# Optimization experiments

Measured on AMD Instinct MI355X. Metric: run time of the kernel, lower is better.

Reference implementation:

```python
import jax, jax.numpy as jnp
import numpy as np

B, T, C, H = 2, 2048, 1024, 16
HS = C // H  # 64
EPS = 1e-5


def layernorm(x, g, b):
    mu = jnp.mean(x, axis=-1, keepdims=True)
    var = jnp.var(x, axis=-1, keepdims=True)
    return (x - mu) * jax.lax.rsqrt(var + EPS) * g + b


def setup_inputs() -> dict:
    key = jax.random.key(0)
    ks = jax.random.split(key, 12)
    s = lambda fan_in: 1.0 / np.sqrt(fan_in)
    inp = {
        'x':  jax.random.normal(ks[0], (B, T, C), dtype=jnp.float32),
        'Wq': jax.random.uniform(ks[1], (H, C, HS), jnp.float32, -s(C), s(C)),
        'Wk': jax.random.uniform(ks[2], (H, C, HS), jnp.float32, -s(C), s(C)),
        'Wv': jax.random.uniform(ks[3], (H, C, HS), jnp.float32, -s(C), s(C)),
        'Wp': jax.random.uniform(ks[4], (C, C), jnp.float32, -s(C), s(C)),
        'bp': jax.random.uniform(ks[5], (C,), jnp.float32, -s(C), s(C)),
        'W1': jax.random.uniform(ks[6], (C, 4 * C), jnp.float32, -s(C), s(C)),
        'b1': jax.random.uniform(ks[7], (4 * C,), jnp.float32, -s(C), s(C)),
        'W2': jax.random.uniform(ks[8], (4 * C, C), jnp.float32, -s(4 * C), s(4 * C)),
        'b2': jax.random.uniform(ks[9], (C,), jnp.float32, -s(4 * C), s(4 * C)),
        'g1': jnp.ones((C,), jnp.float32),
        'be1': jnp.zeros((C,), jnp.float32),
        'g2': jnp.ones((C,), jnp.float32),
        'be2': jnp.zeros((C,), jnp.float32),
    }
    return inp


def block(x, Wq, Wk, Wv, Wp, bp, W1, b1, W2, b2, g1, be1, g2, be2):
    # quirky residual structure: residual is taken from the post-LN tensor
    x = layernorm(x, g1, be1)
    # batched multi-head attention (all heads at once): [B,H,T,HS]
    q = jnp.einsum('btc,hcd->bhtd', x, Wq)
    k = jnp.einsum('btc,hcd->bhtd', x, Wk)
    v = jnp.einsum('btc,hcd->bhtd', x, Wv)
    # NOTE: original scales by full embedding dim C ** -0.5, not head_size
    scores = jnp.einsum('bhtd,bhsd->bhts', q, k) * (C ** -0.5)
    causal = jnp.tril(jnp.ones((T, T), dtype=bool))
    scores = jnp.where(causal, scores, -jnp.inf)
    wei = jax.nn.softmax(scores, axis=-1)  # dropout p=0 in eval
    out = jnp.einsum('bhts,bhsd->bhtd', wei, v)
    out = out.transpose(0, 2, 1, 3).reshape(B, T, C)  # concat heads
    out = out @ Wp + bp
    x = x + out
    x = layernorm(x, g2, be2)
    ff = jax.nn.relu(x @ W1 + b1) @ W2 + b2
    return x + ff


def reference(x, Wq, Wk, Wv, Wp, bp, W1, b1, W2, b2, g1, be1, g2, be2):
    return block(x, Wq, Wk, Wv, Wp, bp, W1, b1, W2, b2, g1, be1, g2, be2)
```

## Files before the change

kernel.cpp:

```cpp
#include <hip/hip_runtime.h>
#include <hip/hip_bf16.h>
#include <cstdint>
#include <cstddef>

typedef __attribute__((ext_vector_type(8))) short short8;
typedef __attribute__((ext_vector_type(4))) float f32x4;
typedef __attribute__((ext_vector_type(16))) float f32x16;
typedef unsigned int u32;
typedef unsigned short u16;

__device__ inline u16 f2b(float x) {
    union { float f; u32 u; } v; v.f = x;
    u32 u = v.u;
    u32 r = (u + 0x7fff + ((u >> 16) & 1)) >> 16;
    return (u16)r;
}
__device__ inline float b2f(u16 h) {
    union { u32 u; float f; } v; v.u = ((u32)h) << 16;
    return v.f;
}
__device__ inline u32 cvtpk(float lo, float hi) {
    u32 r; asm("v_cvt_pk_bf16_f32 %0, %1, %2" : "=v"(r) : "v"(lo), "v"(hi)); return r;
}
__device__ inline float ex2(float x) {
    float r; asm("v_exp_f32 %0, %1" : "=v"(r) : "v"(x)); return r;
}
__device__ inline void gll16(const void* g, void* l) {
    __builtin_amdgcn_global_load_lds(
        (const __attribute__((address_space(1))) void*)g,
        (__attribute__((address_space(3))) void*)l, 16, 0, 0);
}

__global__ __launch_bounds__(256) void repack_qkv_tiled(
    const float* __restrict__ Wq, const float* __restrict__ Wk, const float* __restrict__ Wv,
    u16* __restrict__ out)
{
    __shared__ u16 lds[64 * 72];
    const int tid = threadIdx.x;
    const int c0 = blockIdx.x * 64;
    const int sh = blockIdx.y;
    const int sel = sh >> 4, h = sh & 15;
    const float* W = (sel == 0) ? Wq : (sel == 1) ? Wk : Wv;
    #pragma unroll
    for (int it = 0; it < 4; ++it) {
        int idx = tid + it * 256;
        int c = idx >> 4, d4 = idx & 15;
        float4 v = *reinterpret_cast<const float4*>(&W[((size_t)(h * 1024 + c0 + c)) * 64 + d4 * 4]);
        lds[(d4 * 4 + 0) * 72 + c] = f2b(v.x);
        lds[(d4 * 4 + 1) * 72 + c] = f2b(v.y);
        lds[(d4 * 4 + 2) * 72 + c] = f2b(v.z);
        lds[(d4 * 4 + 3) * 72 + c] = f2b(v.w);
    }
    __syncthreads();
    #pragma unroll
    for (int it = 0; it < 2; ++it) {
        int idx = tid + it * 256;
        int d = idx >> 3, c8 = idx & 7;
        short8 s = *reinterpret_cast<const short8*>(&lds[d * 72 + c8 * 8]);
        *reinterpret_cast<short8*>(&out[((size_t)(sel * 1024 + h * 64 + d)) * 1024 + c0 + c8 * 8]) = s;
    }
}

__global__ __launch_bounds__(256) void trans_tiled(
    const float* __restrict__ in, u16* __restrict__ out, int P, int Q)
{
    __shared__ u16 lds[64 * 72];
    const int tid = threadIdx.x;
    const int p0 = blockIdx.x * 64, q0 = blockIdx.y * 64;
    #pragma unroll
    for (int it = 0; it < 4; ++it) {
        int idx = tid + it * 256;
        int p = idx >> 4, q4 = idx & 15;
        float4 v = *reinterpret_cast<const float4*>(&in[(size_t)(p0 + p) * Q + q0 + q4 * 4]);
        lds[(q4 * 4 + 0) * 72 + p] = f2b(v.x);
        lds[(q4 * 4 + 1) * 72 + p] = f2b(v.y);
        lds[(q4 * 4 + 2) * 72 + p] = f2b(v.z);
        lds[(q4 * 4 + 3) * 72 + p] = f2b(v.w);
    }
    __syncthreads();
    #pragma unroll
    for (int it = 0; it < 2; ++it) {
        int idx = tid + it * 256;
        int q = idx >> 3, p8 = idx & 7;
        short8 s = *reinterpret_cast<const short8*>(&lds[q * 72 + p8 * 8]);
        *reinterpret_cast<short8*>(&out[(size_t)(q0 + q) * P + p0 + p8 * 8]) = s;
    }
}

__global__ __launch_bounds__(256) void vt_kernel(
    const u16* __restrict__ qkv, u16* __restrict__ vt)
{
    __shared__ u16 lds[64 * 72];
    const int tid = threadIdx.x;
    const int s0 = blockIdx.x * 64, h = blockIdx.y, b = blockIdx.z;
    #pragma unroll
    for (int it = 0; it < 2; ++it) {
        int idx = tid + it * 256;
        int s = idx >> 3, d8 = idx & 7;
        short8 kv = *reinterpret_cast<const short8*>(
            &qkv[((size_t)(b * 2048 + s0 + s)) * 3072 + 2048 + h * 64 + d8 * 8]);
        #pragma unroll
        for (int j = 0; j < 8; ++j) lds[(d8 * 8 + j) * 72 + s] = (u16)kv[j];
    }
    __syncthreads();
    #pragma unroll
    for (int it = 0; it < 2; ++it) {
        int idx = tid + it * 256;
        int d = idx >> 3, s8 = idx & 7;
        short8 s = *reinterpret_cast<const short8*>(&lds[d * 72 + s8 * 8]);
        *reinterpret_cast<short8*>(&vt[((size_t)(b * 16 + h) * 64 + d) * 2048 + s0 + s8 * 8]) = s;
    }
}

__global__ __launch_bounds__(256) void ln_kernel(
    const float* __restrict__ x, const float* __restrict__ g, const float* __restrict__ be,
    float* __restrict__ yf, u16* __restrict__ yb)
{
    int row = blockIdx.x;
    const float4 v = reinterpret_cast<const float4*>(x + (size_t)row * 1024)[threadIdx.x];
    float s  = v.x + v.y + v.z + v.w;
    float s2 = v.x * v.x + v.y * v.y + v.z * v.z + v.w * v.w;
    #pragma unroll
    for (int o = 32; o >= 1; o >>= 1) { s += __shfl_xor(s, o); s2 += __shfl_xor(s2, o); }
    __shared__ float red[8];
    int w = threadIdx.x >> 6;
    if ((threadIdx.x & 63) == 0) { red[w] = s; red[4 + w] = s2; }
    __syncthreads();
    s  = red[0] + red[1] + red[2] + red[3];
    s2 = red[4] + red[5] + red[6] + red[7];
    float mu = s * (1.0f / 1024.0f);
    float var = s2 * (1.0f / 1024.0f) - mu * mu;
    float rs = rsqrtf(var + 1e-5f);
    const float4 gg = reinterpret_cast<const float4*>(g)[threadIdx.x];
    const float4 bb = reinterpret_cast<const float4*>(be)[threadIdx.x];
    float4 o;
    o.x = (v.x - mu) * rs * gg.x + bb.x;
    o.y = (v.y - mu) * rs * gg.y + bb.y;
    o.z = (v.z - mu) * rs * gg.z + bb.z;
    o.w = (v.w - mu) * rs * gg.w + bb.w;
    reinterpret_cast<float4*>(yf + (size_t)row * 1024)[threadIdx.x] = o;
    uint2 pk;
    pk.x = (u32)f2b(o.x) | ((u32)f2b(o.y) << 16);
    pk.y = (u32)f2b(o.z) | ((u32)f2b(o.w) << 16);
    reinterpret_cast<uint2*>(yb + (size_t)row * 1024)[threadIdx.x] = pk;
}

template<bool BIAS, bool RELU, bool RESID, bool OUTB>
__global__ __launch_bounds__(256) void gemm_bt(
    const u16* __restrict__ A, int lda,
    const u16* __restrict__ BT, int ldb,
    void* __restrict__ out, int ldo,
    const float* __restrict__ bias,
    const float* __restrict__ resid,
    int K)
{
    __shared__ __align__(16) char smem[64 * 1024];
    const int tid = threadIdx.x;
    const int lane = tid & 63, w = tid >> 6;
    const int wr = w >> 1, wc = w & 1;
    const int l15 = lane & 15, lq = lane >> 4;

    const int nx = gridDim.x;
    const int nwg = nx * gridDim.y;
    int orig = blockIdx.y * nx + blockIdx.x;
    int wgid = orig;
    if ((nwg & 7) == 0) wgid = (orig & 7) * (nwg >> 3) + (orig >> 3);
    const int m0 = (wgid / nx) * 128, n0 = (wgid % nx) * 128;

    auto stage = [&](int kt, int buf) {
        char* As = smem + buf * 32768;
        char* Bs = smem + buf * 32768 + 16384;
        #pragma unroll
        for (int it = 0; it < 4; ++it) {
            int slot = it * 256 + tid;
            int row = slot >> 3, c8 = (slot & 7) ^ (row & 7);
            gll16(A + (size_t)(m0 + row) * lda + kt + c8 * 8, As + (it * 256 + w * 64) * 16);
        }
        #pragma unroll
        for (int it = 0; it < 4; ++it) {
            int slot = it * 256 + tid;
            int row = slot >> 3, c8 = (slot & 7) ^ (row & 7);
            gll16(BT + (size_t)(n0 + row) * ldb + kt + c8 * 8, Bs + (it * 256 + w * 64) * 16);
        }
    };

    f32x4 acc[4][4] = {};
    const int nk = K >> 6;

    stage(0, 0);
    __syncthreads();

    for (int t = 0; t < nk; ++t) {
        const char* As = smem + (t & 1) * 32768;
        const char* Bs = smem + (t & 1) * 32768 + 16384;
        if (t + 1 < nk) stage((t + 1) << 6, (t + 1) & 1);
        #pragma unroll
        for (int kk = 0; kk < 2; ++kk) {
            const int sc = kk * 4 + lq;
            short8 a[4], b[4];
            #pragma unroll
            for (int mi = 0; mi < 4; ++mi) {
                int row = wr * 64 + mi * 16 + l15;
                a[mi] = *reinterpret_cast<const short8*>(As + row * 128 + ((sc ^ (row & 7)) << 4));
            }
            #pragma unroll
            for (int ni = 0; ni < 4; ++ni) {
                int row = wc * 64 + ni * 16 + l15;
                b[ni] = *reinterpret_cast<const short8*>(Bs + row * 128 + ((sc ^ (row & 7)) << 4));
            }
            #pragma unroll
            for (int mi = 0; mi < 4; ++mi)
                #pragma unroll
                for (int ni = 0; ni < 4; ++ni)
                    acc[mi][ni] = __builtin_amdgcn_mfma_f32_16x16x32_bf16(a[mi], b[ni], acc[mi][ni], 0, 0, 0);
        }
        __syncthreads();
    }

    #pragma unroll
    for (int mi = 0; mi < 4; ++mi) {
        #pragma unroll
        for (int ni = 0; ni < 4; ++ni) {
            int col = n0 + wc * 64 + ni * 16 + l15;
            float bv = BIAS ? bias[col] : 0.0f;
            #pragma unroll
            for (int r = 0; r < 4; ++r) {
                int row = m0 + wr * 64 + mi * 16 + lq * 4 + r;
                float v = acc[mi][ni][r] + bv;
                if (RELU) v = v > 0.0f ? v : 0.0f;
                if (RESID) v += resid[(size_t)row * ldo + col];
                if (OUTB) ((u16*)out)[(size_t)row * ldo + col] = f2b(v);
                else      ((float*)out)[(size_t)row * ldo + col] = v;
            }
        }
    }
}

template<bool BIAS, bool RELU, bool OUTB>
__global__ __launch_bounds__(512) void gemm_bt256(
    const u16* __restrict__ A, int lda,
    const u16* __restrict__ BT, int ldb,
    void* __restrict__ out, int ldo,
    const float* __restrict__ bias,
    int K)
{
    __shared__ __align__(16) char smem[128 * 1024];
    const int tid = threadIdx.x;
    const int lane = tid & 63, wid = tid >> 6;
    const int wm = wid >> 2, wn = wid & 3;
    const int l15 = lane & 15, lq = lane >> 4;

    const int nx = gridDim.x;
    const int nwg = nx * gridDim.y;
    int orig = blockIdx.y * nx + blockIdx.x;
    int wgid = orig;
    if ((nwg & 7) == 0) wgid = (orig & 7) * (nwg >> 3) + (orig >> 3);
    const int m0 = (wgid / nx) * 256, n0 = (wgid % nx) * 256;

    auto stage = [&](int kt, int buf) {
        char* As = smem + buf * 65536;
        char* Bs = smem + buf * 65536 + 32768;
        #pragma unroll
        for (int i = 0; i < 4; ++i) {
            int slot = i * 512 + tid;
            int row = slot >> 3, c8 = (slot & 7) ^ (row & 7);
            gll16(A + (size_t)(m0 + row) * lda + kt + c8 * 8, As + (i * 512 + wid * 64) * 16);
        }
        #pragma unroll
        for (int i = 0; i < 4; ++i) {
            int slot = i * 512 + tid;
            int row = slot >> 3, c8 = (slot & 7) ^ (row & 7);
            gll16(BT + (size_t)(n0 + row) * ldb + kt + c8 * 8, Bs + (i * 512 + wid * 64) * 16);
        }
    };

    f32x4 acc[8][4] = {};
    const int nk = K >> 6;

    stage(0, 0);
    asm volatile("s_waitcnt vmcnt(0)" ::: "memory");
    __builtin_amdgcn_s_barrier();

    for (int t = 0; t < nk; ++t) {
        const char* As = smem + (t & 1) * 65536;
        const char* Bs = smem + (t & 1) * 65536 + 32768;
        if (t + 1 < nk) {
            stage((t + 1) << 6, (t + 1) & 1);
            asm volatile("s_waitcnt vmcnt(8)" ::: "memory");
        } else {
            asm volatile("s_waitcnt vmcnt(0)" ::: "memory");
        }
        __builtin_amdgcn_s_barrier();

        #pragma unroll
        for (int kk = 0; kk < 2; ++kk) {
            const int sc = kk * 4 + lq;
            short8 a[8], b[4];
            #pragma unroll
            for (int mi = 0; mi < 8; ++mi) {
                int row = wm * 128 + mi * 16 + l15;
                a[mi] = *reinterpret_cast<const short8*>(As + row * 128 + ((sc ^ (row & 7)) << 4));
            }
            #pragma unroll
            for (int ni = 0; ni < 4; ++ni) {
                int row = wn * 64 + ni * 16 + l15;
                b[ni] = *reinterpret_cast<const short8*>(Bs + row * 128 + ((sc ^ (row & 7)) << 4));
            }
            #pragma unroll
            for (int mi = 0; mi < 8; ++mi)
                #pragma unroll
                for (int ni = 0; ni < 4; ++ni)
                    acc[mi][ni] = __builtin_amdgcn_mfma_f32_16x16x32_bf16(a[mi], b[ni], acc[mi][ni], 0, 0, 0);
        }

        asm volatile("" ::: "memory");
        __builtin_amdgcn_s_barrier();
    }

    #pragma unroll
    for (int mi = 0; mi < 8; ++mi) {
        #pragma unroll
        for (int ni = 0; ni < 4; ++ni) {
            int col = n0 + wn * 64 + ni * 16 + l15;
            float bv = BIAS ? bias[col] : 0.0f;
            #pragma unroll
            for (int r = 0; r < 4; ++r) {
                int row = m0 + wm * 128 + mi * 16 + lq * 4 + r;
                float v = acc[mi][ni][r] + bv;
                if (RELU) v = v > 0.0f ? v : 0.0f;
                if (OUTB) ((u16*)out)[(size_t)row * ldo + col] = f2b(v);
                else      ((float*)out)[(size_t)row * ldo + col] = v;
            }
        }
    }
}

__global__ __launch_bounds__(256, 2) void attn_kernel(
    const u16* __restrict__ qkv, const u16* __restrict__ vt, u16* __restrict__ att)
{
    __shared__ __align__(16) char smem[48 * 1024];
    char* Kb0 = smem;
    char* Kb1 = smem + 8192;
    char* Vb0 = smem + 16384;
    char* Vb1 = smem + 24576;
    char* Ost = smem + 32768;

    const int tid = threadIdx.x, lane = tid & 63, w = tid >> 6;
    const int l31 = lane & 31, hi = lane >> 5;
    const int bh = blockIdx.x;
    const int b = bh >> 4, h = bh & 15;
    const size_t base = (size_t)b * 2048;
    const int kcol = 1024 + h * 64;
    const u16* vtp = vt + (size_t)bh * 64 * 2048;
    const float SC = 0.03125f * 1.44269504f;

    auto stage = [&](int st, char* kb, char* vb) {
        #pragma unroll
        for (int i = 0; i < 2; ++i) {
            int seg = w * 2 + i;
            int slot = seg * 64 + lane;
            int s = slot >> 3, d8p = slot & 7;
            gll16(qkv + (base + st * 64 + s) * 3072 + kcol + ((d8p ^ (s & 7)) * 8),
                  kb + seg * 1024);
            int d = s, s8p = d8p;
            gll16(vtp + (size_t)d * 2048 + st * 64 + ((s8p ^ (d & 7)) * 8),
                  vb + seg * 1024);
        }
    };

    for (int pass = 0; pass < 2; ++pass) {
        const int qbi = pass ? (int)blockIdx.y : 15 - (int)blockIdx.y;
        const int q0w = qbi * 128 + w * 32;
        const int nst = 2 * qbi + 2;
        const int qg = q0w + l31;

        short8 qf[4];
        {
            const u16* qp = qkv + (base + q0w + l31) * 3072 + h * 64 + hi * 8;
            #pragma unroll
            for (int dc = 0; dc < 4; ++dc) {
                short8 q = *reinterpret_cast<const short8*>(qp + dc * 16);
                #pragma unroll
                for (int j = 0; j < 8; j += 2) {
                    u32 pk = cvtpk(b2f((u16)q[j]) * SC, b2f((u16)q[j + 1]) * SC);
                    q[j]     = (short)(pk & 0xffff);
                    q[j + 1] = (short)(pk >> 16);
                }
                qf[dc] = q;
            }
        }

        f32x16 oT[2] = {};
        float m = -1e30f, lsum = 0.0f;

        stage(0, Kb0, Vb0);
        __syncthreads();

        for (int st = 0; st < nst; ++st) {
            char* kb = (st & 1) ? Kb1 : Kb0;
            char* vb = (st & 1) ? Vb1 : Vb0;
            if (st + 1 < nst) stage(st + 1, (st & 1) ? Kb0 : Kb1, (st & 1) ? Vb0 : Vb1);

            f32x16 sa[2] = {};
            #pragma unroll
            for (int dc = 0; dc < 4; ++dc) {
                #pragma unroll
                for (int sb = 0; sb < 2; ++sb) {
                    int s = sb * 32 + l31;
                    int slot = (dc * 2 + hi) ^ (s & 7);
                    short8 kf = *reinterpret_cast<const short8*>(kb + s * 128 + slot * 16);
                    sa[sb] = __builtin_amdgcn_mfma_f32_32x32x16_bf16(kf, qf[dc], sa[sb], 0, 0, 0);
                }
            }

            if (st >= nst - 2) {
                #pragma unroll
                for (int sb = 0; sb < 2; ++sb)
                    #pragma unroll
                    for (int r = 0; r < 16; ++r) {
                        int sg = st * 64 + sb * 32 + (r & 3) + 8 * (r >> 2) + 4 * hi;
                        if (sg > qg) sa[sb][r] = -1e30f;
                    }
            }

            float t8[8];
            #pragma unroll
            for (int i = 0; i < 8; ++i)
                t8[i] = fmaxf(fmaxf(sa[0][i], sa[0][i + 8]), fmaxf(sa[1][i], sa[1][i + 8]));
            float t4a = fmaxf(t8[0], t8[4]), t4b = fmaxf(t8[1], t8[5]);
            float t4c = fmaxf(t8[2], t8[6]), t4d = fmaxf(t8[3], t8[7]);
            float mx = fmaxf(fmaxf(t4a, t4b), fmaxf(t4c, t4d));
            mx = fmaxf(mx, __shfl_xor(mx, 32));

            if (!__all(mx <= m + 8.0f)) {
                float nm = fmaxf(m, mx);
                float sf = ex2(m - nm);
                m = nm;
                lsum *= sf;
                #pragma unroll
                for (int dt = 0; dt < 2; ++dt)
                    #pragma unroll
                    for (int r = 0; r < 16; ++r) oT[dt][r] *= sf;
            }

            #pragma unroll
            for (int sb = 0; sb < 2; ++sb)
                #pragma unroll
                for (int r = 0; r < 16; ++r) sa[sb][r] = ex2(sa[sb][r] - m);
            float s8_[8];
            #pragma unroll
            for (int i = 0; i < 8; ++i)
                s8_[i] = (sa[0][i] + sa[0][i + 8]) + (sa[1][i] + sa[1][i + 8]);
            float s4a = s8_[0] + s8_[4], s4b = s8_[1] + s8_[5];
            float s4c = s8_[2] + s8_[6], s4d = s8_[3] + s8_[7];
            float ps = (s4a + s4b) + (s4c + s4d);
            ps += __shfl_xor(ps, 32);
            lsum += ps;

            u32 pkE[4][2], pkO[4][2];
            #pragma unroll
            for (int sc = 0; sc < 4; ++sc) {
                const int sb = sc >> 1, rb = 8 * (sc & 1);
                #pragma unroll
                for (int c = 0; c < 2; ++c) {
                    pkE[sc][c] = cvtpk(sa[sb][rb + 2 * c], sa[sb][rb + 2 * c + 1]);
                    pkO[sc][c] = cvtpk(sa[sb][rb + 4 + 2 * c], sa[sb][rb + 4 + 2 * c + 1]);
                }
            }

            #pragma unroll
            for (int sc = 0; sc < 4; ++sc) {
                u32 wd[4];
                #pragma unroll
                for (int ww = 0; ww < 4; ++ww) {
                    const int c = ww & 1;
                    u32 own  = hi ? pkO[sc][c] : pkE[sc][c];
                    u32 send = hi ? pkE[sc][c] : pkO[sc][c];
                    u32 ex = (u32)__shfl_xor((int)send, 32);
                    wd[ww] = ((ww >> 1) == hi) ? own : ex;
                }
                union { u32 u[4]; short8 s8; } pb_;
                pb_.u[0] = wd[0]; pb_.u[1] = wd[1]; pb_.u[2] = wd[2]; pb_.u[3] = wd[3];
                #pragma unroll
                for (int dt = 0; dt < 2; ++dt) {
                    int d = dt * 32 + l31;
                    int slot = (sc * 2 + hi) ^ (d & 7);
                    short8 vf = *reinterpret_cast<const short8*>(vb + d * 128 + slot * 16);
                    oT[dt] = __builtin_amdgcn_mfma_f32_32x32x16_bf16(vf, pb_.s8, oT[dt], 0, 0, 0);
                }
            }
            __syncthreads();
        }

        {
            float inv = 1.0f / lsum;
            char* ob = Ost + w * 4096;
            #pragma unroll
            for (int dt = 0; dt < 2; ++dt)
                #pragma unroll
                for (int rp = 0; rp < 8; ++rp) {
                    int r = rp * 2;
                    int d = dt * 32 + (r & 3) + 8 * (r >> 2) + 4 * hi;
                    u32 pk2 = cvtpk(oT[dt][r] * inv, oT[dt][r + 1] * inv);
                    int byte = l31 * 128 + ((((d >> 3) ^ (l31 & 7)) << 4)) + (d & 7) * 2;
                    *reinterpret_cast<u32*>(ob + byte) = pk2;
                }
            int q = lane >> 1, half = lane & 1;
            size_t grow = (base + q0w - w * 32 + (w * 32 + q)) * 1024 + h * 64 + half * 32;
            #pragma unroll
            for (int c = 0; c < 4; ++c) {
                int chunk = half * 4 + c;
                int byte = q * 128 + ((chunk ^ (q & 7)) << 4);
                float4 vv = *reinterpret_cast<const float4*>(ob + byte);
                *reinterpret_cast<float4*>(att + grow + c * 8) = vv;
            }
        }
    }
}

extern "C" void kernel_launch(void* const* d_in, const int* in_sizes, int n_in,
                              void* d_out, int out_size, void* d_ws, size_t ws_size,
                              hipStream_t stream)
{
    const float* x   = (const float*)d_in[0];
    const float* Wq  = (const float*)d_in[1];
    const float* Wk  = (const float*)d_in[2];
    const float* Wv  = (const float*)d_in[3];
    const float* Wp  = (const float*)d_in[4];
    const float* bp  = (const float*)d_in[5];
    const float* W1  = (const float*)d_in[6];
    const float* b1  = (const float*)d_in[7];
    const float* W2  = (const float*)d_in[8];
    const float* b2  = (const float*)d_in[9];
    const float* g1  = (const float*)d_in[10];
    const float* be1 = (const float*)d_in[11];
    const float* g2  = (const float*)d_in[12];
    const float* be2 = (const float*)d_in[13];
    float* out = (float*)d_out;

    char* ws = (char*)d_ws;
    u16*   wqkvT = (u16*)(ws + 0);
    u16*   wpT   = (u16*)(ws + 6291456);
    u16*   w1T   = (u16*)(ws + 8388608);
    u16*   w2T   = (u16*)(ws + 16777216);
    float* xlnF  = (float*)(ws + 25165824);
    u16*   xlnB  = (u16*)(ws + 41943040);
    u16*   qkv   = (u16*)(ws + 50331648);
    float* x2    = (float*)(ws + 50331648);
    u16*   hbuf  = (u16*)(ws + 50331648);
    u16*   attb  = (u16*)(ws + 75497472);
    float* yF    = (float*)(ws + 83886080);
    u16*   vtb   = (u16*)(ws + 83886080);
    u16*   yB    = xlnB;

    repack_qkv_tiled<<<dim3(16, 48), 256, 0, stream>>>(Wq, Wk, Wv, wqkvT);
    trans_tiled<<<dim3(16, 16), 256, 0, stream>>>(Wp, wpT, 1024, 1024);
    trans_tiled<<<dim3(16, 64), 256, 0, stream>>>(W1, w1T, 1024, 4096);
    trans_tiled<<<dim3(64, 16), 256, 0, stream>>>(W2, w2T, 4096, 1024);

    ln_kernel<<<4096, 256, 0, stream>>>(x, g1, be1, xlnF, xlnB);

    gemm_bt256<false, false, true><<<dim3(12, 16), 512, 0, stream>>>(
        xlnB, 1024, wqkvT, 1024, qkv, 3072, nullptr, 1024);

    vt_kernel<<<dim3(32, 16, 2), 256, 0, stream>>>(qkv, vtb);
    attn_kernel<<<dim3(32, 8), 256, 0, stream>>>(qkv, vtb, attb);

    gemm_bt<true, false, true, false><<<dim3(8, 32), 256, 0, stream>>>(
        attb, 1024, wpT, 1024, x2, 1024, bp, xlnF, 1024);

    ln_kernel<<<4096, 256, 0, stream>>>(x2, g2, be2, yF, yB);

    gemm_bt256<true, true, true><<<dim3(16, 16), 512, 0, stream>>>(
        yB, 1024, w1T, 1024, hbuf, 4096, b1, 1024);

    gemm_bt<true, false, true, false><<<dim3(8, 32), 256, 0, stream>>>(
        hbuf, 4096, w2T, 4096, out, 1024, b2, yF, 4096);
}
```

Before: 225.7 us.

## Pre-pack B weights into MFMA fragment order and load from global into registers

```diff
diff --git a/kernel.cpp b/kernel.cpp
--- a/kernel.cpp
+++ b/kernel.cpp
@@ -84,6 +84,35 @@
         int q = idx >> 3, p8 = idx & 7;
         short8 s = *reinterpret_cast<const short8*>(&lds[q * 72 + p8 * 8]);
         *reinterpret_cast<short8*>(&out[(size_t)(q0 + q) * P + p0 + p8 * 8]) = s;
+    }
+}
+
+__global__ __launch_bounds__(256) void trans_fp(
+    const float* __restrict__ in, u16* __restrict__ out, int P, int Q)
+{
+    __shared__ u16 lds[64 * 72];
+    const int tid = threadIdx.x;
+    const int p0 = blockIdx.x * 64, q0 = blockIdx.y * 64;
+    #pragma unroll
+    for (int it = 0; it < 4; ++it) {
+        int idx = tid + it * 256;
+        int p = idx >> 4, q4 = idx & 15;
+        float4 v = *reinterpret_cast<const float4*>(&in[(size_t)(p0 + p) * Q + q0 + q4 * 4]);
+        lds[(q4 * 4 + 0) * 72 + p] = f2b(v.x);
+        lds[(q4 * 4 + 1) * 72 + p] = f2b(v.y);
+        lds[(q4 * 4 + 2) * 72 + p] = f2b(v.z);
+        lds[(q4 * 4 + 3) * 72 + p] = f2b(v.w);
+    }
+    __syncthreads();
+    const int Pd32 = P >> 5;
+    #pragma unroll
+    for (int it = 0; it < 2; ++it) {
+        int idx = tid + it * 256;
+        int q = idx >> 3, p8 = idx & 7;
+        short8 s = *reinterpret_cast<const short8*>(&lds[q * 72 + p8 * 8]);
+        size_t dest = ((size_t)((q0 >> 4) + (q >> 4)) * Pd32 + (p0 >> 5) + (p8 >> 2)) * 512
+                      + (size_t)(p8 & 3) * 128 + (size_t)(q & 15) * 8;
+        *reinterpret_cast<short8*>(out + dest) = s;
     }
 }
 
@@ -148,13 +177,13 @@
 template<bool BIAS, bool RELU, bool RESID, bool OUTB>
 __global__ __launch_bounds__(256) void gemm_bt(
     const u16* __restrict__ A, int lda,
-    const u16* __restrict__ BT, int ldb,
+    const u16* __restrict__ Bfp,
     void* __restrict__ out, int ldo,
     const float* __restrict__ bias,
     const float* __restrict__ resid,
     int K)
 {
-    __shared__ __align__(16) char smem[64 * 1024];
+    __shared__ __align__(16) char smem[32 * 1024];
     const int tid = threadIdx.x;
     const int lane = tid & 63, w = tid >> 6;
     const int wr = w >> 1, wc = w & 1;
@@ -167,53 +196,60 @@
     if ((nwg & 7) == 0) wgid = (orig & 7) * (nwg >> 3) + (orig >> 3);
     const int m0 = (wgid / nx) * 128, n0 = (wgid % nx) * 128;
 
-    auto stage = [&](int kt, int buf) {
-        char* As = smem + buf * 32768;
-        char* Bs = smem + buf * 32768 + 16384;
+    const int n16b = (n0 >> 4) + wc * 4;
+    const int k32n = K >> 5;
+
+    auto stageA = [&](int kt, int buf) {
+        char* As = smem + buf * 16384;
         #pragma unroll
         for (int it = 0; it < 4; ++it) {
             int slot = it * 256 + tid;
             int row = slot >> 3, c8 = (slot & 7) ^ (row & 7);
             gll16(A + (size_t)(m0 + row) * lda + kt + c8 * 8, As + (it * 256 + w * 64) * 16);
         }
-        #pragma unroll
-        for (int it = 0; it < 4; ++it) {
-            int slot = it * 256 + tid;
-            int row = slot >> 3, c8 = (slot & 7) ^ (row & 7);
-            gll16(BT + (size_t)(n0 + row) * ldb + kt + c8 * 8, Bs + (it * 256 + w * 64) * 16);
-        }
     };
 
+    short8 bA[2][4], bB[2][4];
+    auto loadB = [&](short8 (&b)[2][4], int kt) {
+        #pragma unroll
+        for (int kk = 0; kk < 2; ++kk)
+            #pragma unroll
+            for (int ni = 0; ni < 4; ++ni)
+                b[kk][ni] = *reinterpret_cast<const short8*>(
+                    Bfp + (((size_t)(n16b + ni) * k32n + (kt >> 5) + kk) << 9) + lane * 8);
+    };
+
     f32x4 acc[4][4] = {};
-    const int nk = K >> 6;
-
-    stage(0, 0);
-    __syncthreads();
-
-    for (int t = 0; t < nk; ++t) {
-        const char* As = smem + (t & 1) * 32768;
-        const char* Bs = smem + (t & 1) * 32768 + 16384;
-        if (t + 1 < nk) stage((t + 1) << 6, (t + 1) & 1);
+    auto compute = [&](const char* As, short8 (&b)[2][4]) {
         #pragma unroll
         for (int kk = 0; kk < 2; ++kk) {
             const int sc = kk * 4 + lq;
-            short8 a[4], b[4];
+            short8 a[4];
             #pragma unroll
             for (int mi = 0; mi < 4; ++mi) {
                 int row = wr * 64 + mi * 16 + l15;
                 a[mi] = *reinterpret_cast<const short8*>(As + row * 128 + ((sc ^ (row & 7)) << 4));
             }
             #pragma unroll
-            for (int ni = 0; ni < 4; ++ni) {
-                int row = wc * 64 + ni * 16 + l15;
-                b[ni] = *reinterpret_cast<const short8*>(Bs + row * 128 + ((sc ^ (row & 7)) << 4));
-            }
-            #pragma unroll
             for (int mi = 0; mi < 4; ++mi)
                 #pragma unroll
                 for (int ni = 0; ni < 4; ++ni)
-                    acc[mi][ni] = __builtin_amdgcn_mfma_f32_16x16x32_bf16(a[mi], b[ni], acc[mi][ni], 0, 0, 0);
-        }
+                    acc[mi][ni] = __builtin_amdgcn_mfma_f32_16x16x32_bf16(a[mi], b[kk][ni], acc[mi][ni], 0, 0, 0);
+        }
+    };
+
+    const int nk = K >> 6;
+
+    stageA(0, 0);
+    loadB(bA, 0);
+    __syncthreads();
+
+    for (int t = 0; t < nk; t += 2) {
+        if (t + 1 < nk) { stageA((t + 1) << 6, 1); loadB(bB, (t + 1) << 6); }
+        compute(smem, bA);
+        __syncthreads();
+        if (t + 2 < nk) { stageA((t + 2) << 6, 0); loadB(bA, (t + 2) << 6); }
+        compute(smem + 16384, bB);
         __syncthreads();
     }
 
@@ -540,9 +576,9 @@
 
     char* ws = (char*)d_ws;
     u16*   wqkvT = (u16*)(ws + 0);
-    u16*   wpT   = (u16*)(ws + 6291456);
+    u16*   wpFP  = (u16*)(ws + 6291456);
     u16*   w1T   = (u16*)(ws + 8388608);
-    u16*   w2T   = (u16*)(ws + 16777216);
+    u16*   w2FP  = (u16*)(ws + 16777216);
     float* xlnF  = (float*)(ws + 25165824);
     u16*   xlnB  = (u16*)(ws + 41943040);
     u16*   qkv   = (u16*)(ws + 50331648);
@@ -554,9 +590,9 @@
     u16*   yB    = xlnB;
 
     repack_qkv_tiled<<<dim3(16, 48), 256, 0, stream>>>(Wq, Wk, Wv, wqkvT);
-    trans_tiled<<<dim3(16, 16), 256, 0, stream>>>(Wp, wpT, 1024, 1024);
+    trans_fp<<<dim3(16, 16), 256, 0, stream>>>(Wp, wpFP, 1024, 1024);
     trans_tiled<<<dim3(16, 64), 256, 0, stream>>>(W1, w1T, 1024, 4096);
-    trans_tiled<<<dim3(64, 16), 256, 0, stream>>>(W2, w2T, 4096, 1024);
+    trans_fp<<<dim3(64, 16), 256, 0, stream>>>(W2, w2FP, 4096, 1024);
 
     ln_kernel<<<4096, 256, 0, stream>>>(x, g1, be1, xlnF, xlnB);
 
@@ -567,7 +603,7 @@
     attn_kernel<<<dim3(32, 8), 256, 0, stream>>>(qkv, vtb, attb);
 
     gemm_bt<true, false, true, false><<<dim3(8, 32), 256, 0, stream>>>(
-        attb, 1024, wpT, 1024, x2, 1024, bp, xlnF, 1024);
+        attb, 1024, wpFP, x2, 1024, bp, xlnF, 1024);
 
     ln_kernel<<<4096, 256, 0, stream>>>(x2, g2, be2, yF, yB);
 
@@ -575,5 +611,5 @@
         yB, 1024, w1T, 1024, hbuf, 4096, b1, 1024);
 
     gemm_bt<true, false, true, false><<<dim3(8, 32), 256, 0, stream>>>(
-        hbuf, 4096, w2T, 4096, out, 1024, b2, yF, 4096);
-}
+        hbuf, 4096, w2FP, out, 1024, b2, yF, 4096);
+}
```

New measurement: 238.7 us. 1.06x slower.
